# Kernel tuning notes

Measured on AMD Instinct MI355X. Metric: run time of the kernel, lower is better.

The kernel has to match this reference:

```python
import jax, jax.numpy as jnp
import numpy as np

D_MODEL = 1024
N_HEADS = 16
HEAD_DIM = D_MODEL // N_HEADS
BASE = 10000.0


def _rope_cos_sin(seq_len):
    # inv_freq: [head_dim/2]
    inv_freq = 1.0 / (BASE ** (jnp.arange(0, HEAD_DIM, 2, dtype=jnp.float32) / HEAD_DIM))
    t = jnp.arange(seq_len, dtype=jnp.float32)
    freqs = jnp.outer(t, inv_freq)                 # [S, head_dim/2]
    emb = jnp.concatenate([freqs, freqs], axis=-1)  # [S, head_dim]
    return jnp.cos(emb), jnp.sin(emb)


def _rotate_half(x):
    x1, x2 = jnp.split(x, 2, axis=-1)
    return jnp.concatenate([-x2, x1], axis=-1)


def setup_inputs() -> dict:
    key = jax.random.key(0)
    ks = jax.random.split(key, 9)
    B, S, D = 2, 2048, D_MODEL
    sc = 1.0 / np.sqrt(D)
    return {
        "x": jax.random.normal(ks[0], (B, S, D), jnp.float32),
        "Wq": jax.random.normal(ks[1], (D, D), jnp.float32) * sc,
        "bq": jax.random.normal(ks[2], (D,), jnp.float32) * 0.01,
        "Wk": jax.random.normal(ks[3], (D, D), jnp.float32) * sc,
        "bk": jax.random.normal(ks[4], (D,), jnp.float32) * 0.01,
        "Wv": jax.random.normal(ks[5], (D, D), jnp.float32) * sc,
        "bv": jax.random.normal(ks[6], (D,), jnp.float32) * 0.01,
        "Wo": jax.random.normal(ks[7], (D, D), jnp.float32) * sc,
        "bo": jax.random.normal(ks[8], (D,), jnp.float32) * 0.01,
    }


def reference(x, Wq, bq, Wk, bk, Wv, bv, Wo, bo):
    B, S, D = x.shape
    H, Hd = N_HEADS, HEAD_DIM
    # projections (torch Linear: x @ W.T + b), reshape to [B, H, S, Hd]
    def proj(W, b):
        y = jnp.einsum('bsd,ed->bse', x, W) + b
        return y.reshape(B, S, H, Hd).transpose(0, 2, 1, 3)
    q, k, v = proj(Wq, bq), proj(Wk, bk), proj(Wv, bv)
    cos, sin = _rope_cos_sin(S)            # [S, Hd]
    cos = cos[None, None]                   # [1,1,S,Hd]
    sin = sin[None, None]
    q = q * cos + _rotate_half(q) * sin
    k = k * cos + _rotate_half(k) * sin
    scale = jnp.sqrt(jnp.float32(Hd))
    scores = jnp.einsum('bhqd,bhkd->bhqk', q, k) / scale  # [B,H,S,S]
    attn = jax.nn.softmax(scores, axis=-1)
    out = jnp.einsum('bhqk,bhkd->bhqd', attn, v)          # [B,H,S,Hd]
    out = out.transpose(0, 2, 1, 3).reshape(B, S, D)
    return jnp.einsum('bsd,ed->bse', out, Wo) + bo
```

## Files before the change

### kernel.cpp

```cpp
#include <hip/hip_runtime.h>
#include <hip/hip_fp16.h>
#include <math.h>

#define D_MODEL 1024
#define NH 16
#define HD 64
#define SEQ 2048
#define BATCH 2
#define MROWS (BATCH*SEQ)
#define KDIM 1024

typedef unsigned short u16;
typedef __attribute__((ext_vector_type(8))) _Float16 h8;
typedef __attribute__((ext_vector_type(8))) short s8v;
typedef __attribute__((ext_vector_type(4))) float f4v;

#define MFMAH(a, b, c) __builtin_amdgcn_mfma_f32_16x16x32_f16(a, b, c, 0, 0, 0)

__device__ __forceinline__ void gld16(const u16* g, u16* l) {
    __builtin_amdgcn_global_load_lds(
        (const __attribute__((address_space(1))) void*)g,
        (__attribute__((address_space(3))) void*)l, 16, 0, 0);
}

__device__ __forceinline__ u16 f32_to_f16(float f) {
    return __half_as_ushort(__float2half(f));
}

__global__ __launch_bounds__(256)
void convert_f16(const float* __restrict__ x,
                 const float* __restrict__ Wq, const float* __restrict__ Wk,
                 const float* __restrict__ Wv, const float* __restrict__ Wo,
                 u16* __restrict__ xF,
                 u16* __restrict__ WqF, u16* __restrict__ WkF,
                 u16* __restrict__ WvF, u16* __restrict__ WoF,
                 float2* __restrict__ ropeT) {
    int i = blockIdx.x * 256 + threadIdx.x;
    if (i >= (1 << 20)) {
        int idx2 = i - (1 << 20);
        int s  = idx2 >> 5;
        int dd = idx2 & 31;
        float inv = __expf(-(float)dd * 0.2878231366f);
        float ang = (float)s * inv;
        ropeT[idx2] = make_float2(cosf(ang), sinf(ang));
        return;
    }
    const float* src;
    u16* dst;
    int idx;
    if (i < (1 << 19)) {
        src = x; dst = xF; idx = i;
    } else {
        int j = i - (1 << 19);
        int w = j >> 17;
        idx = j & ((1 << 17) - 1);
        switch (w) {
            case 0:  src = Wq; dst = WqF; break;
            case 1:  src = Wk; dst = WkF; break;
            case 2:  src = Wv; dst = WvF; break;
            default: src = Wo; dst = WoF; break;
        }
    }
    float4 a = ((const float4*)src)[idx * 2];
    float4 b = ((const float4*)src)[idx * 2 + 1];
    s8v o;
    o[0] = (short)f32_to_f16(a.x); o[1] = (short)f32_to_f16(a.y);
    o[2] = (short)f32_to_f16(a.z); o[3] = (short)f32_to_f16(a.w);
    o[4] = (short)f32_to_f16(b.x); o[5] = (short)f32_to_f16(b.y);
    o[6] = (short)f32_to_f16(b.z); o[7] = (short)f32_to_f16(b.w);
    ((s8v*)dst)[idx] = o;
}

__global__ __launch_bounds__(256, 2)
void qkv_gemm(const u16* __restrict__ xF, const u16* __restrict__ WqF,
              const u16* __restrict__ WkF, const u16* __restrict__ WvF,
              const float* __restrict__ bq, const float* __restrict__ bk,
              const float* __restrict__ bv,
              const float2* __restrict__ ropeT,
              u16* __restrict__ QF, u16* __restrict__ KF,
              u16* __restrict__ VtF, float* __restrict__ km2) {
    __shared__ __align__(16) u16 SMEM[32768];

    const int t    = threadIdx.x;
    const int w    = t >> 6;
    const int lane = t & 63;
    const int quad = lane >> 4;
    const int l15  = lane & 15;
    const int wr   = w >> 1;
    const int wc   = w & 1;

    const int bid  = blockIdx.x;
    const int xcd  = bid & 7;
    const int j    = bid >> 3;
    const int m0   = (xcd * 4 + (j & 3)) * 128;
    const int yt   = j >> 2;
    const int wsel = yt >> 3;
    const int n0   = (yt & 7) * 128;

    const u16* Bg;
    const float* bias;
    if (wsel == 0)      { Bg = WqF; bias = bq; }
    else if (wsel == 1) { Bg = WkF; bias = bk; }
    else                { Bg = WvF; bias = bv; }

    const int lr = lane >> 3;
    const int lc = (((lane & 7) ^ lr)) * 8;

    f4v acc[4][4];
    #pragma unroll
    for (int i = 0; i < 4; i++)
        #pragma unroll
        for (int jj = 0; jj < 4; jj++)
            acc[i][jj] = (f4v){0.f, 0.f, 0.f, 0.f};

#define STAGE(K0, DB) do {                                                   \
    u16* As_ = SMEM + (DB);                                                  \
    u16* Bs_ = As_ + 8192;                                                   \
    _Pragma("unroll")                                                        \
    for (int jj_ = 0; jj_ < 4; jj_++) {                                      \
        int seg = jj_ * 4 + w;                                               \
        gld16(xF + (size_t)(m0 + seg * 8 + lr) * KDIM + (K0) + lc,           \
              As_ + seg * 512);                                              \
        gld16(Bg + (size_t)(n0 + seg * 8 + lr) * KDIM + (K0) + lc,           \
              Bs_ + seg * 512);                                              \
    }                                                                        \
} while (0)

    STAGE(0, 0);
    __syncthreads();

    int buf = 0;
    for (int k0 = 0; k0 < KDIM; k0 += 64) {
        if (k0 + 64 < KDIM) STAGE(k0 + 64, (buf ^ 1) * 16384);

        const u16* As = SMEM + buf * 16384;
        const u16* Bs = As + 8192;
        #pragma unroll
        for (int kk = 0; kk < 2; kk++) {
            const int swz = ((kk * 4 + quad) ^ (l15 & 7)) << 3;
            h8 a[4], b[4];
            #pragma unroll
            for (int mt = 0; mt < 4; mt++)
                a[mt] = *(const h8*)&As[(wr * 64 + mt * 16 + l15) * 64 + swz];
            #pragma unroll
            for (int nt = 0; nt < 4; nt++)
                b[nt] = *(const h8*)&Bs[(wc * 64 + nt * 16 + l15) * 64 + swz];
            #pragma unroll
            for (int mt = 0; mt < 4; mt++)
                #pragma unroll
                for (int nt = 0; nt < 4; nt++)
                    acc[mt][nt] = MFMAH(a[mt], b[nt], acc[mt][nt]);
        }
        __syncthreads();
        buf ^= 1;
    }
#undef STAGE

    const int bb = m0 >> 11;
    const int s0 = m0 & 2047;
    const int h0 = n0 >> 6;

    if (wsel < 2) {
        u16* OF = (wsel == 0) ? QF : KF;
        float kn_max = 0.f;
        #pragma unroll
        for (int mt = 0; mt < 4; mt++) {
            #pragma unroll
            for (int r = 0; r < 4; r++) {
                int R = wr * 64 + mt * 16 + quad * 4 + r;
                int s = s0 + R;
                float rowsum = 0.f;
                #pragma unroll
                for (int nt = 0; nt < 2; nt++) {
                    int col = wc * 64 + nt * 16 + l15;
                    int n1 = n0 + col;
                    int dd = n1 & 31;
                    float v1 = acc[mt][nt][r]     + bias[n1];
                    float v2 = acc[mt][nt + 2][r] + bias[n1 + 32];
                    float2 cssn = ropeT[(s << 5) | dd];
                    float cs  = cssn.x;
                    float sn  = cssn.y;
                    float r1 = v1 * cs - v2 * sn;
                    float r2 = v2 * cs + v1 * sn;
                    rowsum += v1 * v1 + v2 * v2;
                    SMEM[R * 128 + (((col >> 3) ^ (R & 15)) << 3) + (col & 7)]
                        = f32_to_f16(r1);
                    int col2 = col + 32;
                    SMEM[R * 128 + (((col2 >> 3) ^ (R & 15)) << 3) + (col2 & 7)]
                        = f32_to_f16(r2);
                }
                if (wsel == 1) {
                    rowsum += __shfl_xor(rowsum, 1, 64);
                    rowsum += __shfl_xor(rowsum, 2, 64);
                    rowsum += __shfl_xor(rowsum, 4, 64);
                    rowsum += __shfl_xor(rowsum, 8, 64);
                    kn_max = fmaxf(kn_max, rowsum);
                }
            }
        }
        if (wsel == 1) {
            kn_max = fmaxf(kn_max, __shfl_xor(kn_max, 16, 64));
            kn_max = fmaxf(kn_max, __shfl_xor(kn_max, 32, 64));
            if (lane == 0) atomicMax((int*)km2, __float_as_int(kn_max));
        }
        __syncthreads();
        #pragma unroll
        for (int cc = 0; cc < 8; cc++) {
            int idx  = cc * 256 + t;
            int hl   = idx >> 10;
            int rem  = idx & 1023;
            int R    = rem >> 3;
            int dch  = rem & 7;
            s8v val = *(const s8v*)&SMEM[R * 128 +
                          (((hl * 8 + dch) ^ (R & 15)) << 3)];
            *(s8v*)(OF + (((size_t)bb * NH + h0 + hl) * SEQ + s0 + R) * 64
                       + dch * 8) = val;
        }
    } else {
        #pragma unroll
        for (int mt = 0; mt < 4; mt++) {
            #pragma unroll
            for (int nt = 0; nt < 4; nt++) {
                int n = wc * 64 + nt * 16 + l15;
                float bv_ = bias[n0 + n];
                #pragma unroll
                for (int r = 0; r < 4; r++) {
                    int m = wr * 64 + mt * 16 + quad * 4 + r;
                    float v = acc[mt][nt][r] + bv_;
                    SMEM[n * 128 + (((m >> 3) ^ (n & 15)) << 3) + (m & 7)]
                        = f32_to_f16(v);
                }
            }
        }
        __syncthreads();
        #pragma unroll
        for (int cc = 0; cc < 8; cc++) {
            int idx = cc * 256 + t;
            int n   = idx >> 4;
            int mc  = idx & 15;
            int d   = n & 63;
            int hh  = n >> 6;
            size_t obase = ((size_t)((bb * NH + h0 + hh) * HD + d)) * SEQ + s0;
            s8v val = *(const s8v*)&SMEM[n * 128 + ((mc ^ (n & 15)) << 3)];
            *(s8v*)(VtF + obase + mc * 8) = val;
        }
    }
}

__global__ __launch_bounds__(256, 4)
void flash_attn(const u16* __restrict__ QF, const u16* __restrict__ KF,
                const u16* __restrict__ VtF,
                const float* __restrict__ kmax2,
                u16* __restrict__ AOF) {
    __shared__ __align__(16) u16 KS[2][32 * 72];
    __shared__ __align__(16) u16 VtS[2][64 * 40];

    const int t    = threadIdx.x;
    const int w    = t >> 6;
    const int lane = t & 63;
    const int quad = lane >> 4;
    const int l15  = lane & 15;

    const int bid = blockIdx.x;
    const int xcd = bid & 7;
    const int j   = bid >> 3;
    const int bh  = xcd * 4 + (j & 3);
    const int q0  = (j >> 2) * 64;

    const size_t kvbase = (size_t)bh * SEQ * HD;
    const float km2 = kmax2[0];
    const float C1 = 0.125f * 1.44269504089f;

    h8 qf[2];
    float mb2;
    {
        const u16* qp = QF + kvbase +
            (size_t)(q0 + w * 16 + l15) * HD + quad * 8;
        qf[0] = *(const h8*)qp;
        qf[1] = *(const h8*)(qp + 32);
        float qn2 = 0.f;
        #pragma unroll
        for (int st = 0; st < 2; st++)
            #pragma unroll
            for (int e = 0; e < 8; e++) {
                float v = (float)qf[st][e];
                qn2 += v * v;
            }
        qn2 += __shfl_xor(qn2, 16, 64);
        qn2 += __shfl_xor(qn2, 32, 64);
        mb2 = sqrtf(qn2 * km2) * C1;
    }

    f4v o[4];
    #pragma unroll
    for (int nt = 0; nt < 4; nt++) o[nt] = (f4v){0.f, 0.f, 0.f, 0.f};
    float lsum = 0.f;

    const int krow = t >> 3;
    const int kdc  = (t & 7) * 8;
    const int pkey = (krow & 3) + 8 * ((krow >> 2) & 3) + 4 * (krow >> 4);
    const u16* kgp = KF + kvbase + (size_t)pkey * HD + kdc;
    const int vd   = t >> 2;
    const int vkc  = (t & 3) * 8;
    const int vcol = vkc ^ (((vd >> 3) & 3) << 3);
    const u16* vgp = VtF + (size_t)bh * HD * SEQ + (size_t)vd * SEQ + vkc;

    s8v krg0 = *(const s8v*)(kgp);
    s8v krg1 = *(const s8v*)(kgp + (size_t)32 * HD);
    s8v vrg0 = *(const s8v*)(vgp);
    s8v vrg1 = *(const s8v*)(vgp + 32);

    for (int k0 = 0; k0 < SEQ; k0 += 64) {
        __syncthreads();
        *(s8v*)&KS[0][krow * 72 + kdc] = krg0;
        *(s8v*)&KS[1][krow * 72 + kdc] = krg1;
        *(s8v*)&VtS[0][vd * 40 + vcol] = vrg0;
        *(s8v*)&VtS[1][vd * 40 + vcol] = vrg1;
        if (k0 + 64 < SEQ) {
            const u16* kn = kgp + (size_t)(k0 + 64) * HD;
            krg0 = *(const s8v*)(kn);
            krg1 = *(const s8v*)(kn + (size_t)32 * HD);
            vrg0 = *(const s8v*)(vgp + k0 + 64);
            vrg1 = *(const s8v*)(vgp + k0 + 96);
        }
        __syncthreads();

        #pragma unroll
        for (int sub = 0; sub < 2; sub++) {
            const u16* kb0 = KS[sub] + l15 * 72 + quad * 8;
            const u16* kb1 = KS[sub] + (16 + l15) * 72 + quad * 8;
            h8 kh0 = *(const h8*)kb0, kh1 = *(const h8*)(kb0 + 32);
            h8 kh2 = *(const h8*)kb1, kh3 = *(const h8*)(kb1 + 32);

            f4v sc0 = (f4v){0.f, 0.f, 0.f, 0.f};
            f4v sc1 = (f4v){0.f, 0.f, 0.f, 0.f};
            __builtin_amdgcn_s_setprio(1);
            sc0 = MFMAH(kh0, qf[0], sc0);
            sc0 = MFMAH(kh1, qf[1], sc0);
            sc1 = MFMAH(kh2, qf[0], sc1);
            sc1 = MFMAH(kh3, qf[1], sc1);
            __builtin_amdgcn_s_setprio(0);

            float p[8];
            #pragma unroll
            for (int r = 0; r < 4; r++) {
                p[r]     = __builtin_amdgcn_exp2f(sc0[r] * C1 - mb2);
                p[4 + r] = __builtin_amdgcn_exp2f(sc1[r] * C1 - mb2);
            }
            lsum += ((p[0] + p[1]) + (p[2] + p[3]))
                  + ((p[4] + p[5]) + (p[6] + p[7]));

            h8 pb;
            __half2* pp = (__half2*)&pb;
            pp[0] = __floats2half2_rn(p[0], p[1]);
            pp[1] = __floats2half2_rn(p[2], p[3]);
            pp[2] = __floats2half2_rn(p[4], p[5]);
            pp[3] = __floats2half2_rn(p[6], p[7]);

            __builtin_amdgcn_s_setprio(1);
            #pragma unroll
            for (int nt = 0; nt < 4; nt++) {
                int dim = nt * 16 + l15;
                int voff = dim * 40 + ((quad * 8) ^ (((dim >> 3) & 3) << 3));
                o[nt] = MFMAH(*(const h8*)&VtS[sub][voff], pb, o[nt]);
            }
            __builtin_amdgcn_s_setprio(0);
        }
    }

    lsum += __shfl_xor(lsum, 16, 64);
    lsum += __shfl_xor(lsum, 32, 64);
    float inv_l = 1.0f / lsum;

    const int b = bh >> 4;
    const int h = bh & 15;
    u16* OS = &KS[0][0];
    __syncthreads();
    const int srow = w * 16 + l15;
    #pragma unroll
    for (int nt = 0; nt < 4; nt++) {
        #pragma unroll
        for (int r = 0; r < 4; r++) {
            int d = nt * 16 + quad * 4 + r;
            OS[srow * 64 + (((d >> 3) ^ (srow & 7)) << 3) + (d & 7)]
                = f32_to_f16(o[nt][r] * inv_l);
        }
    }
    __syncthreads();
    #pragma unroll
    for (int cc = 0; cc < 2; cc++) {
        int idx = cc * 256 + t;
        int sr  = idx >> 3;
        int dch = idx & 7;
        s8v val = *(const s8v*)&OS[sr * 64 + ((dch ^ (sr & 7)) << 3)];
        *(s8v*)(AOF + (((size_t)b * SEQ + q0 + sr) * NH + h) * HD + dch * 8)
            = val;
    }
}

__global__ __launch_bounds__(256, 2)
void gemm_out(const u16* __restrict__ AF, const u16* __restrict__ BF,
              const float* __restrict__ bias, float* __restrict__ out) {
    __shared__ __align__(16) u16 SMEM[24576];

    const int t    = threadIdx.x;
    const int w    = t >> 6;
    const int lane = t & 63;
    const int quad = lane >> 4;
    const int l15  = lane & 15;
    const int wr   = w >> 1;
    const int wc   = w & 1;

    const int bid = blockIdx.x;
    const int xcd = bid & 7;
    const int j   = bid >> 3;
    const int m0  = (xcd * 4 + (j & 3)) * 128;
    const int n0  = (j >> 2) * 64;

    const int lr = lane >> 3;
    const int lc = (((lane & 7) ^ lr)) * 8;

    f4v acc[4][2];
    #pragma unroll
    for (int i = 0; i < 4; i++)
        #pragma unroll
        for (int jj = 0; jj < 2; jj++)
            acc[i][jj] = (f4v){0.f, 0.f, 0.f, 0.f};

#define STAGE(K0, DB) do {                                                   \
    u16* As_ = SMEM + (DB);                                                  \
    u16* Bs_ = As_ + 8192;                                                   \
    _Pragma("unroll")                                                        \
    for (int jj_ = 0; jj_ < 4; jj_++) {                                      \
        int seg = jj_ * 4 + w;                                               \
        gld16(AF + (size_t)(m0 + seg * 8 + lr) * KDIM + (K0) + lc,           \
              As_ + seg * 512);                                              \
    }                                                                        \
    _Pragma("unroll")                                                        \
    for (int jj_ = 0; jj_ < 2; jj_++) {                                      \
        int seg = jj_ * 4 + w;                                               \
        gld16(BF + (size_t)(n0 + seg * 8 + lr) * KDIM + (K0) + lc,           \
              Bs_ + seg * 512);                                              \
    }                                                                        \
} while (0)

    STAGE(0, 0);
    __syncthreads();

    int buf = 0;
    for (int k0 = 0; k0 < KDIM; k0 += 64) {
        if (k0 + 64 < KDIM) STAGE(k0 + 64, (buf ^ 1) * 12288);

        const u16* As = SMEM + buf * 12288;
        const u16* Bs = As + 8192;
        #pragma unroll
        for (int kk = 0; kk < 2; kk++) {
            const int swz = ((kk * 4 + quad) ^ (l15 & 7)) << 3;
            h8 a[4], b[2];
            #pragma unroll
            for (int mt = 0; mt < 4; mt++)
                a[mt] = *(const h8*)&As[(wr * 64 + mt * 16 + l15) * 64 + swz];
            #pragma unroll
            for (int nt = 0; nt < 2; nt++)
                b[nt] = *(const h8*)&Bs[(wc * 32 + nt * 16 + l15) * 64 + swz];
            #pragma unroll
            for (int mt = 0; mt < 4; mt++)
                #pragma unroll
                for (int nt = 0; nt < 2; nt++)
                    acc[mt][nt] = MFMAH(a[mt], b[nt], acc[mt][nt]);
        }
        __syncthreads();
        buf ^= 1;
    }
#undef STAGE

    #pragma unroll
    for (int mt = 0; mt < 4; mt++) {
        #pragma unroll
        for (int nt = 0; nt < 2; nt++) {
            int n = n0 + wc * 32 + nt * 16 + l15;
            float bv = bias[n];
            #pragma unroll
            for (int r = 0; r < 4; r++) {
                int m = m0 + wr * 64 + mt * 16 + quad * 4 + r;
                out[(size_t)m * 1024 + n] = acc[mt][nt][r] + bv;
            }
        }
    }
}

extern "C" void kernel_launch(void* const* d_in, const int* in_sizes, int n_in,
                              void* d_out, int out_size, void* d_ws, size_t ws_size,
                              hipStream_t stream) {
    const float* x  = (const float*)d_in[0];
    const float* Wq = (const float*)d_in[1];
    const float* bq = (const float*)d_in[2];
    const float* Wk = (const float*)d_in[3];
    const float* bk = (const float*)d_in[4];
    const float* Wv = (const float*)d_in[5];
    const float* bv = (const float*)d_in[6];
    const float* Wo = (const float*)d_in[7];
    const float* bo = (const float*)d_in[8];
    float* out = (float*)d_out;

    const size_t TEN = (size_t)MROWS * KDIM;
    const size_t WSZ = (size_t)KDIM * KDIM;

    u16* xF  = (u16*)d_ws;
    u16* WqF = xF + TEN;
    u16* WkF = WqF + WSZ;
    u16* WvF = WkF + WSZ;
    u16* WoF = WvF + WSZ;
    u16* QF  = WoF + WSZ;
    u16* KF  = QF + TEN;
    u16* VtF = KF + TEN;
    float* km2 = (float*)(VtF + TEN);
    float2* ropeT = (float2*)(km2 + 4);
    u16* AOF = xF;

    convert_f16<<<4352, 256, 0, stream>>>(x, Wq, Wk, Wv, Wo,
                                          xF, WqF, WkF, WvF, WoF, ropeT);

    hipMemsetAsync(km2, 0, 4, stream);

    qkv_gemm<<<768, 256, 0, stream>>>(xF, WqF, WkF, WvF,
                                      bq, bk, bv, ropeT, QF, KF, VtF, km2);

    flash_attn<<<1024, 256, 0, stream>>>(QF, KF, VtF, km2, AOF);

    gemm_out<<<512, 256, 0, stream>>>(AOF, WoF, bo, out);
}
```

Measured before the change: 208.8 us.

## Process 128 query rows per flash-attention block to reuse K/V tiles

Each flash-attention block now handles two 64-row query groups, so every K and V tile staged in shared memory serves twice as many MFMAs, and the grid is halved. The goal is to cut K/V global loads, shared-memory writes and barriers per unit of work. In exchange it doubles accumulator and Q register use, lowers the launch-bounds occupancy target from 4 to 2 blocks, and leaves fewer blocks to spread across CUs. Shared memory is merged into one buffer so the larger 128-row output staging tile fits.

```diff
diff --git a/kernel.cpp b/kernel.cpp
--- a/kernel.cpp
+++ b/kernel.cpp
@@ -247,13 +247,14 @@
     }
 }
 
-__global__ __launch_bounds__(256, 4)
+__global__ __launch_bounds__(256, 2)
 void flash_attn(const u16* __restrict__ QF, const u16* __restrict__ KF,
                 const u16* __restrict__ VtF,
                 const float* __restrict__ kmax2,
                 u16* __restrict__ AOF) {
-    __shared__ __align__(16) u16 KS[2][32 * 72];
-    __shared__ __align__(16) u16 VtS[2][64 * 40];
+    __shared__ __align__(16) u16 SM[9728];
+    #define KSp(sub) (SM + (sub) * 2304)
+    #define VSp(sub) (SM + 4608 + (sub) * 2560)
 
     const int t    = threadIdx.x;
     const int w    = t >> 6;
@@ -265,36 +266,41 @@
     const int xcd = bid & 7;
     const int j   = bid >> 3;
     const int bh  = xcd * 4 + (j & 3);
-    const int q0  = (j >> 2) * 64;
+    const int q0  = (j >> 2) * 128;
 
     const size_t kvbase = (size_t)bh * SEQ * HD;
     const float km2 = kmax2[0];
     const float C1 = 0.125f * 1.44269504089f;
 
-    h8 qf[2];
-    float mb2;
-    {
+    h8 qf[2][2];
+    float mb2[2];
+    #pragma unroll
+    for (int g = 0; g < 2; g++) {
         const u16* qp = QF + kvbase +
-            (size_t)(q0 + w * 16 + l15) * HD + quad * 8;
-        qf[0] = *(const h8*)qp;
-        qf[1] = *(const h8*)(qp + 32);
+            (size_t)(q0 + g * 64 + w * 16 + l15) * HD + quad * 8;
+        qf[g][0] = *(const h8*)qp;
+        qf[g][1] = *(const h8*)(qp + 32);
         float qn2 = 0.f;
         #pragma unroll
         for (int st = 0; st < 2; st++)
             #pragma unroll
             for (int e = 0; e < 8; e++) {
-                float v = (float)qf[st][e];
+                float v = (float)qf[g][st][e];
                 qn2 += v * v;
             }
         qn2 += __shfl_xor(qn2, 16, 64);
         qn2 += __shfl_xor(qn2, 32, 64);
-        mb2 = sqrtf(qn2 * km2) * C1;
-    }
-
-    f4v o[4];
-    #pragma unroll
-    for (int nt = 0; nt < 4; nt++) o[nt] = (f4v){0.f, 0.f, 0.f, 0.f};
-    float lsum = 0.f;
+        mb2[g] = sqrtf(qn2 * km2) * C1;
+    }
+
+    f4v o[2][4];
+    float lsum[2];
+    #pragma unroll
+    for (int g = 0; g < 2; g++) {
+        #pragma unroll
+        for (int nt = 0; nt < 4; nt++) o[g][nt] = (f4v){0.f, 0.f, 0.f, 0.f};
+        lsum[g] = 0.f;
+    }
 
     const int krow = t >> 3;
     const int kdc  = (t & 7) * 8;
@@ -312,10 +318,10 @@
 
     for (int k0 = 0; k0 < SEQ; k0 += 64) {
         __syncthreads();
-        *(s8v*)&KS[0][krow * 72 + kdc] = krg0;
-        *(s8v*)&KS[1][krow * 72 + kdc] = krg1;
-        *(s8v*)&VtS[0][vd * 40 + vcol] = vrg0;
-        *(s8v*)&VtS[1][vd * 40 + vcol] = vrg1;
+        *(s8v*)&KSp(0)[krow * 72 + kdc] = krg0;
+        *(s8v*)&KSp(1)[krow * 72 + kdc] = krg1;
+        *(s8v*)&VSp(0)[vd * 40 + vcol]  = vrg0;
+        *(s8v*)&VSp(1)[vd * 40 + vcol]  = vrg1;
         if (k0 + 64 < SEQ) {
             const u16* kn = kgp + (size_t)(k0 + 64) * HD;
             krg0 = *(const s8v*)(kn);
@@ -327,68 +333,81 @@
 
         #pragma unroll
         for (int sub = 0; sub < 2; sub++) {
-            const u16* kb0 = KS[sub] + l15 * 72 + quad * 8;
-            const u16* kb1 = KS[sub] + (16 + l15) * 72 + quad * 8;
+            const u16* kb0 = KSp(sub) + l15 * 72 + quad * 8;
+            const u16* kb1 = KSp(sub) + (16 + l15) * 72 + quad * 8;
             h8 kh0 = *(const h8*)kb0, kh1 = *(const h8*)(kb0 + 32);
             h8 kh2 = *(const h8*)kb1, kh3 = *(const h8*)(kb1 + 32);
 
-            f4v sc0 = (f4v){0.f, 0.f, 0.f, 0.f};
-            f4v sc1 = (f4v){0.f, 0.f, 0.f, 0.f};
-            __builtin_amdgcn_s_setprio(1);
-            sc0 = MFMAH(kh0, qf[0], sc0);
-            sc0 = MFMAH(kh1, qf[1], sc0);
-            sc1 = MFMAH(kh2, qf[0], sc1);
-            sc1 = MFMAH(kh3, qf[1], sc1);
-            __builtin_amdgcn_s_setprio(0);
-
-            float p[8];
-            #pragma unroll
-            for (int r = 0; r < 4; r++) {
-                p[r]     = __builtin_amdgcn_exp2f(sc0[r] * C1 - mb2);
-                p[4 + r] = __builtin_amdgcn_exp2f(sc1[r] * C1 - mb2);
-            }
-            lsum += ((p[0] + p[1]) + (p[2] + p[3]))
-                  + ((p[4] + p[5]) + (p[6] + p[7]));
-
-            h8 pb;
-            __half2* pp = (__half2*)&pb;
-            pp[0] = __floats2half2_rn(p[0], p[1]);
-            pp[1] = __floats2half2_rn(p[2], p[3]);
-            pp[2] = __floats2half2_rn(p[4], p[5]);
-            pp[3] = __floats2half2_rn(p[6], p[7]);
+            h8 pb[2];
+            #pragma unroll
+            for (int g = 0; g < 2; g++) {
+                f4v sc0 = (f4v){0.f, 0.f, 0.f, 0.f};
+                f4v sc1 = (f4v){0.f, 0.f, 0.f, 0.f};
+                __builtin_amdgcn_s_setprio(1);
+                sc0 = MFMAH(kh0, qf[g][0], sc0);
+                sc0 = MFMAH(kh1, qf[g][1], sc0);
+                sc1 = MFMAH(kh2, qf[g][0], sc1);
+                sc1 = MFMAH(kh3, qf[g][1], sc1);
+                __builtin_amdgcn_s_setprio(0);
+
+                float p[8];
+                #pragma unroll
+                for (int r = 0; r < 4; r++) {
+                    p[r]     = __builtin_amdgcn_exp2f(sc0[r] * C1 - mb2[g]);
+                    p[4 + r] = __builtin_amdgcn_exp2f(sc1[r] * C1 - mb2[g]);
+                }
+                lsum[g] += ((p[0] + p[1]) + (p[2] + p[3]))
+                         + ((p[4] + p[5]) + (p[6] + p[7]));
+
+                __half2* pp = (__half2*)&pb[g];
+                pp[0] = __floats2half2_rn(p[0], p[1]);
+                pp[1] = __floats2half2_rn(p[2], p[3]);
+                pp[2] = __floats2half2_rn(p[4], p[5]);
+                pp[3] = __floats2half2_rn(p[6], p[7]);
+            }
 
             __builtin_amdgcn_s_setprio(1);
             #pragma unroll
             for (int nt = 0; nt < 4; nt++) {
                 int dim = nt * 16 + l15;
                 int voff = dim * 40 + ((quad * 8) ^ (((dim >> 3) & 3) << 3));
-                o[nt] = MFMAH(*(const h8*)&VtS[sub][voff], pb, o[nt]);
+                h8 vf = *(const h8*)&VSp(sub)[voff];
+                o[0][nt] = MFMAH(vf, pb[0], o[0][nt]);
+                o[1][nt] = MFMAH(vf, pb[1], o[1][nt]);
             }
             __builtin_amdgcn_s_setprio(0);
         }
     }
 
-    lsum += __shfl_xor(lsum, 16, 64);
-    lsum += __shfl_xor(lsum, 32, 64);
-    float inv_l = 1.0f / lsum;
+    float inv_l[2];
+    #pragma unroll
+    for (int g = 0; g < 2; g++) {
+        float l = lsum[g];
+        l += __shfl_xor(l, 16, 64);
+        l += __shfl_xor(l, 32, 64);
+        inv_l[g] = 1.0f / l;
+    }
 
     const int b = bh >> 4;
     const int h = bh & 15;
-    u16* OS = &KS[0][0];
+    u16* OS = SM;
     __syncthreads();
-    const int srow = w * 16 + l15;
-    #pragma unroll
-    for (int nt = 0; nt < 4; nt++) {
-        #pragma unroll
-        for (int r = 0; r < 4; r++) {
-            int d = nt * 16 + quad * 4 + r;
-            OS[srow * 64 + (((d >> 3) ^ (srow & 7)) << 3) + (d & 7)]
-                = f32_to_f16(o[nt][r] * inv_l);
+    #pragma unroll
+    for (int g = 0; g < 2; g++) {
+        const int srow = g * 64 + w * 16 + l15;
+        #pragma unroll
+        for (int nt = 0; nt < 4; nt++) {
+            #pragma unroll
+            for (int r = 0; r < 4; r++) {
+                int d = nt * 16 + quad * 4 + r;
+                OS[srow * 64 + (((d >> 3) ^ (srow & 7)) << 3) + (d & 7)]
+                    = f32_to_f16(o[g][nt][r] * inv_l[g]);
+            }
         }
     }
     __syncthreads();
     #pragma unroll
-    for (int cc = 0; cc < 2; cc++) {
+    for (int cc = 0; cc < 4; cc++) {
         int idx = cc * 256 + t;
         int sr  = idx >> 3;
         int dch = idx & 7;
@@ -396,6 +415,8 @@
         *(s8v*)(AOF + (((size_t)b * SEQ + q0 + sr) * NH + h) * HD + dch * 8)
             = val;
     }
+    #undef KSp
+    #undef VSp
 }
 
 __global__ __launch_bounds__(256, 2)
@@ -526,7 +547,7 @@
     qkv_gemm<<<768, 256, 0, stream>>>(xF, WqF, WkF, WvF,
                                       bq, bk, bv, ropeT, QF, KF, VtF, km2);
 
-    flash_attn<<<1024, 256, 0, stream>>>(QF, KF, VtF, km2, AOF);
+    flash_attn<<<512, 256, 0, stream>>>(QF, KF, VtF, km2, AOF);
 
     gemm_out<<<512, 256, 0, stream>>>(AOF, WoF, bo, out);
 }
```

New measurement: 198.9 us. 1.05x faster.
